# Kernel optimization log

Hardware: AMD Instinct MI355X
Metric: run time of the kernel (lower is better)

Reference implementation:

```python
import jax, jax.numpy as jnp
import numpy as np


def setup_inputs() -> dict:
    key = jax.random.key(0)
    k1, k2, k3, k4 = jax.random.split(key, 4)
    B, Nq, Nk, D = 8, 2048, 2048, 768
    return {
        "query": jax.random.normal(k1, (B, Nq, D), dtype=jnp.float32),
        "key": jax.random.normal(k2, (Nk, D), dtype=jnp.float32),
        "x": jax.random.normal(k3, (B, Nk, D), dtype=jnp.float32),
        "W": jax.random.normal(k4, (D, D), dtype=jnp.float32) * (1.0 / np.sqrt(D)),
        "b": jnp.zeros((D,), dtype=jnp.float32),
    }


def reference(query, key, x, W, b):
    # Linear projection: [B,Nq,dk] @ W^T + b -> [B,Nq,dq]
    query_proj = jnp.einsum("bqd,ed->bqe", query, W) + b
    # tensordot over dim_query: [B,Nq,dq] x [Nk,dq] -> [B,Nq,Nk]
    score = jnp.einsum("bqe,ke->bqk", query_proj, key)
    attn = jax.nn.softmax(score, axis=-1)
    # bmm: [B,Nq,Nk] @ [B,Nk,Dv] -> [B,Nq,Dv]
    out = jnp.einsum("bqk,bkd->bqd", attn, x)
    return (out, attn)
```

## Files before the change

### kernel.cpp

```cpp
#include <hip/hip_runtime.h>

typedef short s16x8 __attribute__((ext_vector_type(8)));
typedef _Float16 h16x8 __attribute__((ext_vector_type(8)));
typedef float f32x4 __attribute__((ext_vector_type(4)));

__device__ __forceinline__ unsigned short f2bf(float f) {
    unsigned int u = __builtin_bit_cast(unsigned int, f);
    u += 0x7FFFu + ((u >> 16) & 1u);
    return (unsigned short)(u >> 16);
}
__device__ __forceinline__ float bf2f(unsigned short h) {
    unsigned int u = ((unsigned int)h) << 16;
    return __builtin_bit_cast(float, u);
}
__device__ __forceinline__ unsigned short f2h(float f) {
    _Float16 h = (_Float16)f;
    return __builtin_bit_cast(unsigned short, h);
}
__device__ __forceinline__ float h2f(unsigned short u) {
    return (float)__builtin_bit_cast(_Float16, u);
}

__device__ __forceinline__ int swz(int row, int kbyte) {
    return (row * 64 + kbyte) ^ (((row >> 1) & 3) << 4);
}

__device__ __forceinline__ void gl16(const void* g, void* l) {
    __builtin_amdgcn_global_load_lds(
        (__attribute__((address_space(1))) void*)(g),
        (__attribute__((address_space(3))) void*)(l), 16, 0, 0);
}

#define STG(ptr, rowbase, tt, bufp, slot) do {                                      \
    gl16((ptr) + (long)((rowbase) + sl) * K + (tt) * 64 + koff,                     \
         &lds[bufp][slot][(unsigned)t * 8]);                                        \
    gl16((ptr) + (long)((rowbase) + 64 + sl) * K + (tt) * 64 + koff,                \
         &lds[bufp][slot][4096u + (unsigned)t * 8]);                                \
} while (0)

#define LDA(qi_) do {                                                               \
    const char* ba_ = (const char*)&lds[bp][qi_][0];                                \
    _Pragma("unroll")                                                               \
    for (int ks_ = 0; ks_ < 2; ++ks_)                                               \
        _Pragma("unroll")                                                           \
        for (int f_ = 0; f_ < 4; ++f_) {                                            \
            const int row_ = wm * 64 + f_ * 16 + lr;                                \
            af[ks_][f_] = *(const h16x8*)(ba_ + row_ * 128 +                        \
                            ((ks_ * 64 + kg16) ^ ((row_ & 7) << 4)));               \
        }                                                                           \
} while (0)

#define LDB(dst_, qj_) do {                                                         \
    const char* bb_ = (const char*)&lds[bp][2 + (qj_)][0];                          \
    _Pragma("unroll")                                                               \
    for (int ks_ = 0; ks_ < 2; ++ks_)                                               \
        _Pragma("unroll")                                                           \
        for (int g_ = 0; g_ < 2; ++g_) {                                            \
            const int row_ = wn * 32 + g_ * 16 + lr;                                \
            dst_[ks_][g_] = *(const h16x8*)(bb_ + row_ * 128 +                      \
                            ((ks_ * 64 + kg16) ^ ((row_ & 7) << 4)));               \
        }                                                                           \
} while (0)

#define SYNCV(VMSTR) do {                                                           \
    asm volatile("s_waitcnt vmcnt(" VMSTR ")" ::: "memory");                        \
    __builtin_amdgcn_s_barrier();                                                   \
    __builtin_amdgcn_sched_barrier(0);                                              \
} while (0)

#define MM(qi_, qj_, bfv_) do {                                                     \
    __builtin_amdgcn_s_setprio(1);                                                  \
    _Pragma("unroll")                                                               \
    for (int ks_ = 0; ks_ < 2; ++ks_)                                               \
        _Pragma("unroll")                                                           \
        for (int f_ = 0; f_ < 4; ++f_)                                              \
            _Pragma("unroll")                                                       \
            for (int g_ = 0; g_ < 2; ++g_)                                          \
                acc[qi_][qj_][f_][g_] = __builtin_amdgcn_mfma_f32_16x16x32_f16(     \
                    af[ks_][f_], bfv_[ks_][g_], acc[qi_][qj_][f_][g_], 0, 0, 0);    \
    __builtin_amdgcn_s_setprio(0);                                                  \
    __builtin_amdgcn_s_barrier();                                                   \
    __builtin_amdgcn_sched_barrier(0);                                              \
} while (0)

__global__ __launch_bounds__(512, 2) void score_8ph(
    const unsigned short* __restrict__ A, const unsigned short* __restrict__ Bm,
    const float* __restrict__ bias, float* __restrict__ C,
    int M, int N, int K, int nbx)
{
    __shared__ unsigned short lds[2][4][8192];

    const int bid = blockIdx.x;
    const int cpx = gridDim.x >> 3;
    const int sw  = (bid & 7) * cpx + (bid >> 3);
    const int m0 = (sw / nbx) * 256, n0 = (sw % nbx) * 256;

    const int t = threadIdx.x;
    const int l = t & 63, w = t >> 6;
    const int wm = w >> 2, wn = w & 3;
    const int lr = l & 15;
    const int kg16 = (l >> 4) * 16;

    const int sl   = w * 8 + (l >> 3);
    const int koff = ((l & 7) ^ (sl & 7)) * 8;

    h16x8 af[2][4], bf0[2][2], bf1[2][2];
    f32x4 acc[2][2][4][2];
    #pragma unroll
    for (int a = 0; a < 2; ++a)
        #pragma unroll
        for (int b = 0; b < 2; ++b)
            #pragma unroll
            for (int c = 0; c < 4; ++c)
                #pragma unroll
                for (int d = 0; d < 2; ++d)
                    acc[a][b][c][d] = (f32x4){0.f, 0.f, 0.f, 0.f};

    const int nt = K >> 6;

    STG(A,  m0,       0, 0, 0);
    STG(Bm, n0,       0, 0, 2);
    STG(Bm, n0 + 128, 0, 0, 3);
    STG(A,  m0 + 128, 0, 0, 1);
    STG(A,  m0,       1, 1, 0);
    STG(Bm, n0,       1, 1, 2);
    asm volatile("s_waitcnt vmcnt(8)" ::: "memory");
    __builtin_amdgcn_s_barrier();
    __builtin_amdgcn_sched_barrier(0);

    int tau = 0;
    for (; tau < nt - 2; ++tau) {
        const int bp = tau & 1;
        LDA(0); LDB(bf0, 0);
        STG(Bm, n0 + 128, tau + 1, bp ^ 1, 3);
        SYNCV("8");
        MM(0, 0, bf0);
        LDB(bf1, 1);
        STG(A, m0 + 128, tau + 1, bp ^ 1, 1);
        SYNCV("8");
        MM(0, 1, bf1);
        LDA(1);
        STG(A, m0, tau + 2, bp, 0);
        SYNCV("10");
        MM(1, 1, bf1);
        STG(Bm, n0, tau + 2, bp, 2);
        SYNCV("8");
        MM(1, 0, bf0);
    }
    {
        const int bp = tau & 1;
        LDA(0); LDB(bf0, 0);
        STG(Bm, n0 + 128, tau + 1, bp ^ 1, 3);
        SYNCV("8");
        MM(0, 0, bf0);
        LDB(bf1, 1);
        STG(A, m0 + 128, tau + 1, bp ^ 1, 1);
        SYNCV("8");
        MM(0, 1, bf1);
        LDA(1);
        SYNCV("8");
        MM(1, 1, bf1);
        SYNCV("4");
        MM(1, 0, bf0);
        ++tau;
    }
    {
        const int bp = tau & 1;
        LDA(0); LDB(bf0, 0);
        SYNCV("2");
        MM(0, 0, bf0);
        LDB(bf1, 1);
        SYNCV("0");
        MM(0, 1, bf1);
        LDA(1);
        SYNCV("0");
        MM(1, 1, bf1);
        SYNCV("0");
        MM(1, 0, bf0);
    }

    #pragma unroll
    for (int qi = 0; qi < 2; ++qi)
        #pragma unroll
        for (int qj = 0; qj < 2; ++qj)
            #pragma unroll
            for (int f = 0; f < 4; ++f)
                #pragma unroll
                for (int g = 0; g < 2; ++g) {
                    const int row = m0 + qi * 128 + wm * 64 + f * 16 + (l >> 4) * 4;
                    const int col = n0 + qj * 128 + wn * 32 + g * 16 + lr;
                    const float badd = bias[col];
                    #pragma unroll
                    for (int r = 0; r < 4; ++r)
                        C[(long)(row + r) * N + col] = acc[qi][qj][f][g][r] + badd;
                }
}

__global__ __launch_bounds__(256, 1) void pv_2ph(
    const unsigned short* __restrict__ A, const unsigned short* __restrict__ Bm,
    float* __restrict__ C, int M, int N, int K,
    long strideA, long strideB, long strideC)
{
    __shared__ unsigned short lds[2][2][128 * 64];

    const int bz = blockIdx.z;
    const unsigned short* Ab = A  + (long)bz * strideA;
    const unsigned short* Bb = Bm + (long)bz * strideB;
    float* Cb = C + (long)bz * strideC;
    const int m0 = blockIdx.x * 128, n0 = blockIdx.y * 128;

    const int t = threadIdx.x;
    const int l = t & 63, w = t >> 6;
    const int rm = (w >> 1) * 64, cn = (w & 1) * 64;
    const int lr = l & 15;
    const int kg16 = (l >> 4) * 16;

    const int jrow   = l >> 3;
    const int srcoff = ((l & 7) ^ jrow) << 3;

    const unsigned short* gA = Ab + (long)(m0 + jrow) * K + srcoff;
    const unsigned short* gB = Bb + (long)(n0 + jrow) * K + srcoff;

    f32x4 acc[4][4];
    #pragma unroll
    for (int i = 0; i < 4; ++i)
        #pragma unroll
        for (int j = 0; j < 4; ++j)
            acc[i][j] = (f32x4){0.f, 0.f, 0.f, 0.f};

    const int nt = K >> 6;
    #pragma unroll
    for (int i = 0; i < 4; ++i) {
        const int c = w * 4 + i;
        gl16(gA + (long)(8 * c) * K, &lds[0][0][c * 512]);
        gl16(gB + (long)(8 * c) * K, &lds[0][1][c * 512]);
    }
    __syncthreads();

    int p = 0;
    for (int it = 0; it < nt; ++it) {
        if (it + 1 < nt) {
            const unsigned short* nA = gA + (it + 1) * 64;
            const unsigned short* nB = gB + (it + 1) * 64;
            #pragma unroll
            for (int i = 0; i < 4; ++i) {
                const int c = w * 4 + i;
                gl16(nA + (long)(8 * c) * K, &lds[p ^ 1][0][c * 512]);
                gl16(nB + (long)(8 * c) * K, &lds[p ^ 1][1][c * 512]);
            }
        }
        const char* baseA = (const char*)&lds[p][0][0];
        const char* baseB = (const char*)&lds[p][1][0];
        h16x8 af[2][4], bf[2][4];
        #pragma unroll
        for (int ks = 0; ks < 2; ++ks)
            #pragma unroll
            for (int mi = 0; mi < 4; ++mi) {
                const int row = rm + mi * 16 + lr;
                af[ks][mi] = *(const h16x8*)(baseA + row * 128 +
                                ((ks * 64 + kg16) ^ ((row & 7) << 4)));
            }
        #pragma unroll
        for (int ks = 0; ks < 2; ++ks)
            #pragma unroll
            for (int nj = 0; nj < 4; ++nj) {
                const int row = cn + nj * 16 + lr;
                bf[ks][nj] = *(const h16x8*)(baseB + row * 128 +
                                ((ks * 64 + kg16) ^ ((row & 7) << 4)));
            }
        #pragma unroll
        for (int ks = 0; ks < 2; ++ks)
            #pragma unroll
            for (int mi = 0; mi < 4; ++mi)
                #pragma unroll
                for (int nj = 0; nj < 4; ++nj)
                    acc[mi][nj] = __builtin_amdgcn_mfma_f32_16x16x32_f16(
                        af[ks][mi], bf[ks][nj], acc[mi][nj], 0, 0, 0);
        __syncthreads();
        p ^= 1;
    }

    #pragma unroll
    for (int mi = 0; mi < 4; ++mi) {
        #pragma unroll
        for (int nj = 0; nj < 4; ++nj) {
            const int row = m0 + rm + mi * 16 + (l >> 4) * 4;
            const int col = n0 + cn + nj * 16 + lr;
            #pragma unroll
            for (int r = 0; r < 4; ++r)
                Cb[(long)(row + r) * N + col] = acc[mi][nj][r];
        }
    }
}

template<int SPLIT, bool TRANSB, bool BIAS>
__global__ __launch_bounds__(256, 1) void mfma_gemm(
    const float* __restrict__ A, const float* __restrict__ Bsrc,
    const float* __restrict__ bias, float* __restrict__ C,
    int M, int N, int K, long strideA, long strideB, long strideC)
{
    constexpr int NB = (SPLIT > 1) ? 2 : 1;
    __shared__ unsigned short sA[NB][128 * 32];
    __shared__ unsigned short sB[NB][128 * 32];

    const int t  = threadIdx.x;
    const int bz = blockIdx.z;
    const float* Ab = A    + (long)bz * strideA;
    const float* Bb = Bsrc + (long)bz * strideB;
    float*       Cb = C    + (long)bz * strideC;
    const int m0 = blockIdx.y * 128;
    const int n0 = blockIdx.x * 128;

    const int l  = t & 63, w = t >> 6;
    const int rm = (w >> 1) * 64;
    const int cn = (w & 1) * 64;
    const int lr = l & 15;
    const int kg = (l >> 4) * 16;

    const int srow = t >> 1;
    const int skh  = (t & 1) * 16;
    const int s_ = t & 15;
    const int kp = t >> 4;

    f32x4 acc[4][4];
    #pragma unroll
    for (int i = 0; i < 4; ++i)
        #pragma unroll
        for (int j = 0; j < 4; ++j)
            acc[i][j] = (f32x4){0.f, 0.f, 0.f, 0.f};

    for (int kt = 0; kt < K; kt += 32) {
        {
            const float* p = &Ab[(long)(m0 + srow) * K + kt + skh];
            float f[16];
            #pragma unroll
            for (int q = 0; q < 4; ++q) {
                const float4 v = *(const float4*)(p + 4 * q);
                f[4*q+0] = v.x; f[4*q+1] = v.y; f[4*q+2] = v.z; f[4*q+3] = v.w;
            }
            s16x8 h0, h1, l0, l1;
            #pragma unroll
            for (int q = 0; q < 8; ++q) {
                unsigned short h = f2bf(f[q]);      h0[q] = (short)h;
                if (SPLIT > 1) l0[q] = (short)f2bf(f[q] - bf2f(h));
                unsigned short g = f2bf(f[8 + q]);  h1[q] = (short)g;
                if (SPLIT > 1) l1[q] = (short)f2bf(f[8 + q] - bf2f(g));
            }
            *(s16x8*)((char*)sA[0] + swz(srow, skh * 2))      = h0;
            *(s16x8*)((char*)sA[0] + swz(srow, skh * 2 + 16)) = h1;
            if (SPLIT > 1) {
                *(s16x8*)((char*)sA[1] + swz(srow, skh * 2))      = l0;
                *(s16x8*)((char*)sA[1] + swz(srow, skh * 2 + 16)) = l1;
            }
        }
        if (!TRANSB) {
            const float* p = &Bb[(long)(n0 + srow) * K + kt + skh];
            float f[16];
            #pragma unroll
            for (int q = 0; q < 4; ++q) {
                const float4 v = *(const float4*)(p + 4 * q);
                f[4*q+0] = v.x; f[4*q+1] = v.y; f[4*q+2] = v.z; f[4*q+3] = v.w;
            }
            s16x8 h0, h1, l0, l1;
            #pragma unroll
            for (int q = 0; q < 8; ++q) {
                unsigned short h = f2bf(f[q]);      h0[q] = (short)h;
                if (SPLIT > 1) l0[q] = (short)f2bf(f[q] - bf2f(h));
                unsigned short g = f2bf(f[8 + q]);  h1[q] = (short)g;
                if (SPLIT > 1) l1[q] = (short)f2bf(f[8 + q] - bf2f(g));
            }
            *(s16x8*)((char*)sB[0] + swz(srow, skh * 2))      = h0;
            *(s16x8*)((char*)sB[0] + swz(srow, skh * 2 + 16)) = h1;
            if (SPLIT > 1) {
                *(s16x8*)((char*)sB[1] + swz(srow, skh * 2))      = l0;
                *(s16x8*)((char*)sB[1] + swz(srow, skh * 2 + 16)) = l1;
            }
        } else {
            const float* r0 = &Bb[(long)(kt + 2 * kp) * N + n0 + s_ * 8];
            const float* r1 = r0 + N;
            float a0[8], a1[8];
            {
                const float4 u0 = *(const float4*)(r0);
                const float4 u1 = *(const float4*)(r0 + 4);
                const float4 v0 = *(const float4*)(r1);
                const float4 v1 = *(const float4*)(r1 + 4);
                a0[0]=u0.x;a0[1]=u0.y;a0[2]=u0.z;a0[3]=u0.w;
                a0[4]=u1.x;a0[5]=u1.y;a0[6]=u1.z;a0[7]=u1.w;
                a1[0]=v0.x;a1[1]=v0.y;a1[2]=v0.z;a1[3]=v0.w;
                a1[4]=v1.x;a1[5]=v1.y;a1[6]=v1.z;a1[7]=v1.w;
            }
            #pragma unroll
            for (int j = 0; j < 8; ++j) {
                const int i  = (j + s_) & 7;
                const int nl = s_ * 8 + i;
                const unsigned int val =
                    (unsigned int)f2bf(a0[i]) | ((unsigned int)f2bf(a1[i]) << 16);
                *(unsigned int*)((char*)sB[0] + swz(nl, 4 * kp)) = val;
            }
        }
        __syncthreads();

        s16x8 ah[4], bh[4];
        #pragma unroll
        for (int mi = 0; mi < 4; ++mi)
            ah[mi] = *(const s16x8*)((const char*)sA[0] + swz(rm + mi * 16 + lr, kg));
        #pragma unroll
        for (int nj = 0; nj < 4; ++nj)
            bh[nj] = *(const s16x8*)((const char*)sB[0] + swz(cn + nj * 16 + lr, kg));
        #pragma unroll
        for (int mi = 0; mi < 4; ++mi)
            #pragma unroll
            for (int nj = 0; nj < 4; ++nj)
                acc[mi][nj] = __builtin_amdgcn_mfma_f32_16x16x32_bf16(
                    ah[mi], bh[nj], acc[mi][nj], 0, 0, 0);
        if (SPLIT > 1) {
            s16x8 al[4], bl[4];
            #pragma unroll
            for (int mi = 0; mi < 4; ++mi)
                al[mi] = *(const s16x8*)((const char*)sA[1] + swz(rm + mi * 16 + lr, kg));
            #pragma unroll
            for (int mi = 0; mi < 4; ++mi)
                #pragma unroll
                for (int nj = 0; nj < 4; ++nj)
                    acc[mi][nj] = __builtin_amdgcn_mfma_f32_16x16x32_bf16(
                        al[mi], bh[nj], acc[mi][nj], 0, 0, 0);
            #pragma unroll
            for (int nj = 0; nj < 4; ++nj)
                bl[nj] = *(const s16x8*)((const char*)sB[1] + swz(cn + nj * 16 + lr, kg));
            #pragma unroll
            for (int mi = 0; mi < 4; ++mi)
                #pragma unroll
                for (int nj = 0; nj < 4; ++nj)
                    acc[mi][nj] = __builtin_amdgcn_mfma_f32_16x16x32_bf16(
                        ah[mi], bl[nj], acc[mi][nj], 0, 0, 0);
        }
        __syncthreads();
    }

    #pragma unroll
    for (int mi = 0; mi < 4; ++mi) {
        #pragma unroll
        for (int nj = 0; nj < 4; ++nj) {
            const int row = m0 + rm + mi * 16 + (l >> 4) * 4;
            const int col = n0 + cn + nj * 16 + lr;
            const float badd = BIAS ? bias[col] : 0.f;
            #pragma unroll
            for (int r = 0; r < 4; ++r)
                Cb[(long)(row + r) * N + col] = acc[mi][nj][r] + badd;
        }
    }
}

__global__ __launch_bounds__(256, 1) void score_gemm(
    const unsigned short* __restrict__ Ah, const unsigned short* __restrict__ Al,
    const unsigned short* __restrict__ Bh, const unsigned short* __restrict__ Bl,
    const float* __restrict__ bias, float* __restrict__ C,
    int M, int N, int K, int nbx)
{
    __shared__ unsigned short sAh[128 * 32];
    __shared__ unsigned short sBh[128 * 32];
    __shared__ unsigned short sAl[128 * 32];
    __shared__ unsigned short sBl[128 * 32];

    const int bid = blockIdx.x;
    const int cpx = gridDim.x >> 3;
    const int sw  = (bid & 7) * cpx + (bid >> 3);
    const int mb  = sw / nbx, nb = sw % nbx;
    const int m0 = mb * 128, n0 = nb * 128;

    const int t = threadIdx.x;
    const int l = t & 63, w = t >> 6;
    const int rm = (w >> 1) * 64;
    const int cn = (w & 1) * 64;
    const int lr = l & 15;
    const int kg = (l >> 4) * 16;

    const int r0 = 2 * w, r1 = 2 * w + 1;
    const int rowS0 = 16 * r0 + (l >> 2);
    const int rowS1 = 16 * r1 + (l >> 2);
    const int h0 = (l & 3) ^ ((rowS0 >> 1) & 3);
    const int h1 = (l & 3) ^ ((rowS1 >> 1) & 3);

    const unsigned short* gAh0 = Ah + (long)(m0 + rowS0) * K + 8 * h0;
    const unsigned short* gAh1 = Ah + (long)(m0 + rowS1) * K + 8 * h1;
    const unsigned short* gAl0 = Al + (long)(m0 + rowS0) * K + 8 * h0;
    const unsigned short* gAl1 = Al + (long)(m0 + rowS1) * K + 8 * h1;
    const unsigned short* gBh0 = Bh + (long)(n0 + rowS0) * K + 8 * h0;
    const unsigned short* gBh1 = Bh + (long)(n0 + rowS1) * K + 8 * h1;
    const unsigned short* gBl0 = Bl + (long)(n0 + rowS0) * K + 8 * h0;
    const unsigned short* gBl1 = Bl + (long)(n0 + rowS1) * K + 8 * h1;

    unsigned short* dA0 = &sAh[r0 * 512];
    unsigned short* dA1 = &sAh[r1 * 512];
    unsigned short* dAl0 = &sAl[r0 * 512];
    unsigned short* dAl1 = &sAl[r1 * 512];
    unsigned short* dB0 = &sBh[r0 * 512];
    unsigned short* dB1 = &sBh[r1 * 512];
    unsigned short* dBl0 = &sBl[r0 * 512];
    unsigned short* dBl1 = &sBl[r1 * 512];

    f32x4 acc[4][4];
    #pragma unroll
    for (int i = 0; i < 4; ++i)
        #pragma unroll
        for (int j = 0; j < 4; ++j)
            acc[i][j] = (f32x4){0.f, 0.f, 0.f, 0.f};

    const int nk = K >> 5;
    for (int it = 0; it < nk; ++it) {
        gl16(gAh0, dA0);  gl16(gAh1, dA1);
        gl16(gBh0, dB0);  gl16(gBh1, dB1);
        gl16(gAl0, dAl0); gl16(gAl1, dAl1);
        gl16(gBl0, dBl0); gl16(gBl1, dBl1);
        gAh0 += 32; gAh1 += 32; gAl0 += 32; gAl1 += 32;
        gBh0 += 32; gBh1 += 32; gBl0 += 32; gBl1 += 32;
        __syncthreads();

        s16x8 ah[4], bh[4];
        #pragma unroll
        for (int mi = 0; mi < 4; ++mi)
            ah[mi] = *(const s16x8*)((const char*)sAh + swz(rm + mi * 16 + lr, kg));
        #pragma unroll
        for (int nj = 0; nj < 4; ++nj)
            bh[nj] = *(const s16x8*)((const char*)sBh + swz(cn + nj * 16 + lr, kg));
        #pragma unroll
        for (int mi = 0; mi < 4; ++mi)
            #pragma unroll
            for (int nj = 0; nj < 4; ++nj)
                acc[mi][nj] = __builtin_amdgcn_mfma_f32_16x16x32_bf16(
                    ah[mi], bh[nj], acc[mi][nj], 0, 0, 0);
        s16x8 al[4], bl[4];
        #pragma unroll
        for (int mi = 0; mi < 4; ++mi)
            al[mi] = *(const s16x8*)((const char*)sAl + swz(rm + mi * 16 + lr, kg));
        #pragma unroll
        for (int mi = 0; mi < 4; ++mi)
            #pragma unroll
            for (int nj = 0; nj < 4; ++nj)
                acc[mi][nj] = __builtin_amdgcn_mfma_f32_16x16x32_bf16(
                    al[mi], bh[nj], acc[mi][nj], 0, 0, 0);
        #pragma unroll
        for (int nj = 0; nj < 4; ++nj)
            bl[nj] = *(const s16x8*)((const char*)sBl + swz(cn + nj * 16 + lr, kg));
        #pragma unroll
        for (int mi = 0; mi < 4; ++mi)
            #pragma unroll
            for (int nj = 0; nj < 4; ++nj)
                acc[mi][nj] = __builtin_amdgcn_mfma_f32_16x16x32_bf16(
                    ah[mi], bl[nj], acc[mi][nj], 0, 0, 0);
        __syncthreads();
    }

    #pragma unroll
    for (int mi = 0; mi < 4; ++mi) {
        #pragma unroll
        for (int nj = 0; nj < 4; ++nj) {
            const int row = m0 + rm + mi * 16 + (l >> 4) * 4;
            const int col = n0 + cn + nj * 16 + lr;
            const float badd = bias[col];
            #pragma unroll
            for (int r = 0; r < 4; ++r)
                C[(long)(row + r) * N + col] = acc[mi][nj][r] + badd;
        }
    }
}

__global__ __launch_bounds__(256, 1) void out_gemm(
    const float* __restrict__ A32, const unsigned short* __restrict__ B16,
    float* __restrict__ C, int M, int N, int K,
    long strideA, long strideB, long strideC)
{
    __shared__ unsigned short sA[128 * 32];
    __shared__ unsigned short sB[128 * 32];

    const int bz = blockIdx.z;
    const float* Ab = A32 + (long)bz * strideA;
    const unsigned short* Bb = B16 + (long)bz * strideB;
    float* Cb = C + (long)bz * strideC;
    const int m0 = blockIdx.x * 128;
    const int n0 = blockIdx.y * 128;

    const int t = threadIdx.x;
    const int l = t & 63, w = t >> 6;
    const int rm = (w >> 1) * 64;
    const int cn = (w & 1) * 64;
    const int lr = l & 15;
    const int kg = (l >> 4) * 16;

    const int r0 = 2 * w, r1 = 2 * w + 1;
    const int rowS0 = 16 * r0 + (l >> 2);
    const int rowS1 = 16 * r1 + (l >> 2);
    const int h0 = (l & 3) ^ ((rowS0 >> 1) & 3);
    const int h1 = (l & 3) ^ ((rowS1 >> 1) & 3);
    const unsigned short* gB0 = Bb + (long)(n0 + rowS0) * K + 8 * h0;
    const unsigned short* gB1 = Bb + (long)(n0 + rowS1) * K + 8 * h1;
    unsigned short* dB0 = &sB[r0 * 512];
    unsigned short* dB1 = &sB[r1 * 512];

    const int srow = t >> 1;
    const int skh  = (t & 1) * 16;
    const float* gA = &Ab[(long)(m0 + srow) * K + skh];

    f32x4 acc[4][4];
    #pragma unroll
    for (int i = 0; i < 4; ++i)
        #pragma unroll
        for (int j = 0; j < 4; ++j)
            acc[i][j] = (f32x4){0.f, 0.f, 0.f, 0.f};

    const int nk = K >> 5;
    for (int it = 0; it < nk; ++it) {
        gl16(gB0, dB0); gl16(gB1, dB1);
        gB0 += 32; gB1 += 32;
        {
            float f[16];
            #pragma unroll
            for (int q = 0; q < 4; ++q) {
                const float4 v = *(const float4*)(gA + 4 * q);
                f[4*q+0] = v.x; f[4*q+1] = v.y; f[4*q+2] = v.z; f[4*q+3] = v.w;
            }
            gA += 32;
            s16x8 v0, v1;
            #pragma unroll
            for (int q = 0; q < 8; ++q) {
                v0[q] = (short)f2bf(f[q]);
                v1[q] = (short)f2bf(f[8 + q]);
            }
            *(s16x8*)((char*)sA + swz(srow, skh * 2))      = v0;
            *(s16x8*)((char*)sA + swz(srow, skh * 2 + 16)) = v1;
        }
        __syncthreads();

        s16x8 ah[4], bh[4];
        #pragma unroll
        for (int mi = 0; mi < 4; ++mi)
            ah[mi] = *(const s16x8*)((const char*)sA + swz(rm + mi * 16 + lr, kg));
        #pragma unroll
        for (int nj = 0; nj < 4; ++nj)
            bh[nj] = *(const s16x8*)((const char*)sB + swz(cn + nj * 16 + lr, kg));
        #pragma unroll
        for (int mi = 0; mi < 4; ++mi)
            #pragma unroll
            for (int nj = 0; nj < 4; ++nj)
                acc[mi][nj] = __builtin_amdgcn_mfma_f32_16x16x32_bf16(
                    ah[mi], bh[nj], acc[mi][nj], 0, 0, 0);
        __syncthreads();
    }

    #pragma unroll
    for (int mi = 0; mi < 4; ++mi) {
        #pragma unroll
        for (int nj = 0; nj < 4; ++nj) {
            const int row = m0 + rm + mi * 16 + (l >> 4) * 4;
            const int col = n0 + cn + nj * 16 + lr;
            #pragma unroll
            for (int r = 0; r < 4; ++r)
                Cb[(long)(row + r) * N + col] = acc[mi][nj][r];
        }
    }
}

template<int MODE>
__global__ __launch_bounds__(256) void transpose64(
    const float* __restrict__ in, void* __restrict__ outv,
    int R, int Cc, long sIn, long sOut)
{
    __shared__ float tl[64][65];
    const int z = blockIdx.z;
    const float* ib = in + (long)z * sIn;
    const int r0 = blockIdx.x * 64, c0 = blockIdx.y * 64;
    const int t = threadIdx.x;
    const int lrr = t >> 4, lc = (t & 15) * 4;
    #pragma unroll
    for (int p = 0; p < 4; ++p) {
        const float4 v = *(const float4*)&ib[(long)(r0 + lrr + 16 * p) * Cc + c0 + lc];
        tl[lrr + 16 * p][lc + 0] = v.x; tl[lrr + 16 * p][lc + 1] = v.y;
        tl[lrr + 16 * p][lc + 2] = v.z; tl[lrr + 16 * p][lc + 3] = v.w;
    }
    __syncthreads();
    #pragma unroll
    for (int p = 0; p < 4; ++p) {
        const int orow = c0 + lrr + 16 * p;
        const int ocol = r0 + lc;
        const float a = tl[lc + 0][lrr + 16 * p];
        const float b = tl[lc + 1][lrr + 16 * p];
        const float c = tl[lc + 2][lrr + 16 * p];
        const float d = tl[lc + 3][lrr + 16 * p];
        if (MODE == 1) {
            ushort4 u = { f2bf(a), f2bf(b), f2bf(c), f2bf(d) };
            *(ushort4*)((unsigned short*)outv + (long)z * sOut + (long)orow * R + ocol) = u;
        } else if (MODE == 2) {
            ushort4 u = { f2h(a), f2h(b), f2h(c), f2h(d) };
            *(ushort4*)((unsigned short*)outv + (long)z * sOut + (long)orow * R + ocol) = u;
        } else {
            float4 u = { a, b, c, d };
            *(float4*)((float*)outv + (long)z * sOut + (long)orow * R + ocol) = u;
        }
    }
}

__global__ __launch_bounds__(256) void convert_hilo(
    const float* __restrict__ src, unsigned short* __restrict__ hi,
    unsigned short* __restrict__ lo, long n8)
{
    for (long i = (long)blockIdx.x * blockDim.x + threadIdx.x; i < n8;
         i += (long)gridDim.x * blockDim.x) {
        const float4 a = *(const float4*)&src[i * 8];
        const float4 b = *(const float4*)&src[i * 8 + 4];
        const float f[8] = { a.x, a.y, a.z, a.w, b.x, b.y, b.z, b.w };
        s16x8 h, lv;
        #pragma unroll
        for (int q = 0; q < 8; ++q) {
            const unsigned short hh = f2bf(f[q]);
            h[q]  = (short)hh;
            lv[q] = (short)f2bf(f[q] - bf2f(hh));
        }
        *(s16x8*)&hi[i * 8] = h;
        *(s16x8*)&lo[i * 8] = lv;
    }
}

__global__ __launch_bounds__(256) void convert_q_ilv(
    const float* __restrict__ src, unsigned short* __restrict__ dst,
    int kd8, long n8)
{
    const int Kd = kd8 * 8;
    for (long i = (long)blockIdx.x * blockDim.x + threadIdx.x; i < n8;
         i += (long)gridDim.x * blockDim.x) {
        const long row = i / kd8;
        const int  col = (int)(i - row * kd8) * 8;
        const float4 a = *(const float4*)&src[i * 8];
        const float4 b = *(const float4*)&src[i * 8 + 4];
        const float f[8] = { a.x, a.y, a.z, a.w, b.x, b.y, b.z, b.w };
        s16x8 h, lv;
        #pragma unroll
        for (int q = 0; q < 8; ++q) {
            const unsigned short hh = f2h(f[q]);
            h[q]  = (short)hh;
            lv[q] = (short)f2h(f[q] - h2f(hh));
        }
        unsigned short* dr = dst + row * (long)(2 * Kd);
        *(s16x8*)&dr[col]      = h;
        *(s16x8*)&dr[Kd + col] = lv;
    }
}

__global__ __launch_bounds__(256) void convert_kw_dup(
    const float* __restrict__ src, unsigned short* __restrict__ dst,
    int kd8, long n8)
{
    const int Kd = kd8 * 8;
    for (long i = (long)blockIdx.x * blockDim.x + threadIdx.x; i < n8;
         i += (long)gridDim.x * blockDim.x) {
        const long row = i / kd8;
        const int  col = (int)(i - row * kd8) * 8;
        const float4 a = *(const float4*)&src[i * 8];
        const float4 b = *(const float4*)&src[i * 8 + 4];
        const float f[8] = { a.x, a.y, a.z, a.w, b.x, b.y, b.z, b.w };
        s16x8 h;
        #pragma unroll
        for (int q = 0; q < 8; ++q) h[q] = (short)f2h(f[q]);
        unsigned short* dr = dst + row * (long)(2 * Kd);
        *(s16x8*)&dr[col]      = h;
        *(s16x8*)&dr[Kd + col] = h;
    }
}

__global__ __launch_bounds__(256) void bk_dot(
    const float* __restrict__ key, const float* __restrict__ b,
    float* __restrict__ bk, int D)
{
    const int row = blockIdx.x * 4 + (threadIdx.x >> 6);
    const int l = threadIdx.x & 63;
    const float* kr = key + (long)row * D;
    float s = 0.f;
    for (int e = l; e < D; e += 64) s += kr[e] * b[e];
    #pragma unroll
    for (int off = 32; off > 0; off >>= 1) s += __shfl_xor(s, off);
    if (l == 0) bk[row] = s;
}

__global__ __launch_bounds__(256) void softmax_f16(
    float* __restrict__ S, unsigned short* __restrict__ S16, int cols)
{
    const long row = blockIdx.x;
    float* p = S + row * (long)cols;
    unsigned short* p16 = S16 + row * (long)cols;
    const int t = threadIdx.x;
    const int wid = t >> 6;
    const int base = t * 8;

    const float4 a = *(const float4*)&p[base];
    const float4 b = *(const float4*)&p[base + 4];
    float vals[8] = { a.x, a.y, a.z, a.w, b.x, b.y, b.z, b.w };
    float m = -INFINITY;
    #pragma unroll
    for (int i = 0; i < 8; ++i) m = fmaxf(m, vals[i]);
    #pragma unroll
    for (int off = 32; off > 0; off >>= 1)
        m = fmaxf(m, __shfl_xor(m, off));
    __shared__ float smax[4], ssum[4];
    if ((t & 63) == 0) smax[wid] = m;
    __syncthreads();
    m = fmaxf(fmaxf(smax[0], smax[1]), fmaxf(smax[2], smax[3]));

    float s = 0.f;
    #pragma unroll
    for (int i = 0; i < 8; ++i) {
        vals[i] = __expf(vals[i] - m);
        s += vals[i];
    }
    #pragma unroll
    for (int off = 32; off > 0; off >>= 1)
        s += __shfl_xor(s, off);
    if ((t & 63) == 0) ssum[wid] = s;
    __syncthreads();
    s = (ssum[0] + ssum[1]) + (ssum[2] + ssum[3]);
    const float inv = 1.0f / s;

    float4 o0, o1;
    o0.x = vals[0]*inv; o0.y = vals[1]*inv; o0.z = vals[2]*inv; o0.w = vals[3]*inv;
    o1.x = vals[4]*inv; o1.y = vals[5]*inv; o1.z = vals[6]*inv; o1.w = vals[7]*inv;
    *(float4*)&p[base]     = o0;
    *(float4*)&p[base + 4] = o1;
    s16x8 h;
    h[0]=(short)f2h(o0.x); h[1]=(short)f2h(o0.y); h[2]=(short)f2h(o0.z); h[3]=(short)f2h(o0.w);
    h[4]=(short)f2h(o1.x); h[5]=(short)f2h(o1.y); h[6]=(short)f2h(o1.z); h[7]=(short)f2h(o1.w);
    *(s16x8*)&p16[base] = h;
}

__global__ __launch_bounds__(256) void softmax_rows(float* __restrict__ S, int cols)
{
    const long row = blockIdx.x;
    float* p = S + row * (long)cols;
    const int t = threadIdx.x;
    const int wid = t >> 6;

    float vals[8];
    float m = -INFINITY;
    #pragma unroll
    for (int i = 0; i < 8; ++i) {
        vals[i] = p[t + i * 256];
        m = fmaxf(m, vals[i]);
    }
    #pragma unroll
    for (int off = 32; off > 0; off >>= 1)
        m = fmaxf(m, __shfl_xor(m, off));
    __shared__ float smax[4], ssum[4];
    if ((t & 63) == 0) smax[wid] = m;
    __syncthreads();
    m = fmaxf(fmaxf(smax[0], smax[1]), fmaxf(smax[2], smax[3]));

    float s = 0.f;
    #pragma unroll
    for (int i = 0; i < 8; ++i) {
        vals[i] = __expf(vals[i] - m);
        s += vals[i];
    }
    #pragma unroll
    for (int off = 32; off > 0; off >>= 1)
        s += __shfl_xor(s, off);
    if ((t & 63) == 0) ssum[wid] = s;
    __syncthreads();
    s = (ssum[0] + ssum[1]) + (ssum[2] + ssum[3]);
    const float inv = 1.0f / s;
    #pragma unroll
    for (int i = 0; i < 8; ++i)
        p[t + i * 256] = vals[i] * inv;
}

extern "C" void kernel_launch(void* const* d_in, const int* in_sizes, int n_in,
                              void* d_out, int out_size, void* d_ws, size_t ws_size,
                              hipStream_t stream)
{
    const float* query = (const float*)d_in[0];
    const float* key   = (const float*)d_in[1];
    const float* x     = (const float*)d_in[2];
    const float* W     = (const float*)d_in[3];
    const float* bias  = (const float*)d_in[4];

    const int D  = in_sizes[4];
    const int Nk = in_sizes[1] / D;
    const int B  = in_sizes[2] / (Nk * D);
    const int Nq = in_sizes[0] / (B * D);

    float* out  = (float*)d_out;
    float* attn = out + (long)B * Nq * D;

    const long nQ  = (long)B * Nq * D;
    const long nKW = (long)Nk * D;
    const long nX  = (long)B * Nk * D;
    const int  M   = B * Nq;
    const int  K2  = 2 * D;

    const size_t xTb    = (size_t)nX * 2;
    const size_t kwDupB = (size_t)Nk * K2 * 2;
    const size_t bkB    = (size_t)Nk * 4;
    const size_t atb1   = (size_t)Nq * Nk * 2;
    const size_t fixedB = xTb + kwDupB + bkB;
    const size_t qLob   = (size_t)nQ * 2;
    const size_t wsMid  = xTb + qLob;

    int g = 0;
    if (ws_size >= fixedB + 2 * atb1) {
        g = (int)((ws_size - fixedB) / atb1);
        if (g > B) g = B;
    }

    if (g >= 2) {
        unsigned short* qIlv  = (unsigned short*)out;
        unsigned short* xT     = (unsigned short*)d_ws;
        unsigned short* kwDup  = (unsigned short*)((char*)d_ws + xTb);
        float*          bk     = (float*)((char*)d_ws + xTb + kwDupB);
        unsigned short* attn16 = (unsigned short*)((char*)d_ws + fixedB);
        float* Wt  = attn;
        float* KWf = attn + 1048576;

        dim3 gtw(D / 64, D / 64, 1);
        transpose64<0><<<gtw, 256, 0, stream>>>(W, Wt, D, D, 0L, 0L);
        dim3 gkw(D / 128, Nk / 128, 1);
        mfma_gemm<3, false, false><<<gkw, 256, 0, stream>>>(
            key, Wt, nullptr, KWf, Nk, D, D, 0L, 0L, 0L);
        convert_kw_dup<<<768, 256, 0, stream>>>(KWf, kwDup, D / 8, nKW / 8);
        bk_dot<<<Nk / 4, 256, 0, stream>>>(key, bias, bk, D);
        convert_q_ilv<<<2048, 256, 0, stream>>>(query, qIlv, D / 8, nQ / 8);
        dim3 gtx(Nk / 64, D / 64, B);
        transpose64<2><<<gtx, 256, 0, stream>>>(
            x, xT, Nk, D, (long)Nk * D, (long)D * Nk);

        const int nbx = Nk / 256;
        const int nwg = (M / 256) * nbx;
        score_8ph<<<nwg, 512, 0, stream>>>(
            qIlv, kwDup, bk, attn, M, Nk, K2, nbx);

        for (int b0 = 0; b0 < B; b0 += g) {
            const int gb = (b0 + g <= B) ? g : (B - b0);
            softmax_f16<<<gb * Nq, 256, 0, stream>>>(
                attn + (long)b0 * Nq * Nk, attn16, Nk);
            dim3 go(Nq / 128, D / 128, gb);
            pv_2ph<<<go, 256, 0, stream>>>(
                attn16, xT + (long)b0 * D * Nk, out + (long)b0 * Nq * D,
                Nq, D, Nk, (long)Nq * Nk, (long)D * Nk, (long)Nq * D);
        }
    } else if (ws_size >= wsMid) {
        unsigned short* q_hi  = (unsigned short*)out;
        unsigned short* KW_hi = q_hi + nQ;
        unsigned short* KW_lo = KW_hi + nKW;
        float*          bk    = (float*)(KW_lo + nKW);
        unsigned short* q_lo  = (unsigned short*)d_ws;
        unsigned short* xT    = q_lo + nQ;
        float* Wt  = attn;
        float* KWf = attn + 1048576;

        dim3 gtw(D / 64, D / 64, 1);
        transpose64<0><<<gtw, 256, 0, stream>>>(W, Wt, D, D, 0L, 0L);
        dim3 gkw(D / 128, Nk / 128, 1);
        mfma_gemm<3, false, false><<<gkw, 256, 0, stream>>>(
            key, Wt, nullptr, KWf, Nk, D, D, 0L, 0L, 0L);
        convert_hilo<<<768, 256, 0, stream>>>(KWf, KW_hi, KW_lo, nKW / 8);
        bk_dot<<<Nk / 4, 256, 0, stream>>>(key, bias, bk, D);
        convert_hilo<<<2048, 256, 0, stream>>>(query, q_hi, q_lo, nQ / 8);
        dim3 gtx(Nk / 64, D / 64, B);
        transpose64<1><<<gtx, 256, 0, stream>>>(
            x, xT, Nk, D, (long)Nk * D, (long)D * Nk);
        const int nbx = Nk / 128;
        const int nwg = (B * Nq / 128) * nbx;
        score_gemm<<<nwg, 256, 0, stream>>>(
            q_hi, q_lo, KW_hi, KW_lo, bk, attn, B * Nq, Nk, D, nbx);
        softmax_rows<<<B * Nq, 256, 0, stream>>>(attn, Nk);
        dim3 go(Nq / 128, D / 128, B);
        out_gemm<<<go, 256, 0, stream>>>(
            attn, xT, out, Nq, D, Nk, (long)Nq * Nk, (long)D * Nk, (long)Nq * D);
    } else {
        float* qp = out;
        dim3 g1(D / 128, (B * Nq) / 128, 1);
        mfma_gemm<3, false, true><<<g1, 256, 0, stream>>>(
            query, W, bias, qp, B * Nq, D, D, 0L, 0L, 0L);
        dim3 g2(Nk / 128, Nq / 128, B);
        mfma_gemm<3, false, false><<<g2, 256, 0, stream>>>(
            qp, key, nullptr, attn, Nq, Nk, D, (long)Nq * D, 0L, (long)Nq * Nk);
        softmax_rows<<<B * Nq, 256, 0, stream>>>(attn, Nk);
        dim3 g4(D / 128, Nq / 128, B);
        mfma_gemm<1, true, false><<<g4, 256, 0, stream>>>(
            attn, x, nullptr, out, Nq, D, Nk, (long)Nq * Nk, (long)Nk * D, (long)Nq * D);
    }
}
```

Before: 336.8 us.

## Emit fp16 scores, fuse softmax in place, and process batches in two groups

Adds a new path, used when the workspace is large enough and B==8. It runs the score GEMM in two 4-batch groups and writes the scores as fp16 into a workspace slot instead of fp32 into attn. A new softmax kernel reads the fp16 slot, writes fp32 attn, and overwrites the slot with fp16 probabilities for the PV GEMM. This replaces the fp32 score write plus fp32 read in softmax with smaller fp16 traffic. The score kernel's global-load pipeline is also re-timed: next-stage loads are issued earlier and there is one vmcnt wait per iteration instead of a wait at each phase. The risk is reduced precision from rounding scores to fp16 before the softmax, and possible load/LDS-buffer hazards under the new prefetch ordering.

Measured after the change: 311.4 us. 1.08x faster.

```diff
diff --git a/kernel.cpp b/kernel.cpp
--- a/kernel.cpp
+++ b/kernel.cpp
@@ -62,8 +62,7 @@
         }                                                                           \
 } while (0)
 
-#define SYNCV(VMSTR) do {                                                           \
-    asm volatile("s_waitcnt vmcnt(" VMSTR ")" ::: "memory");                        \
+#define BARR() do {                                                                 \
     __builtin_amdgcn_s_barrier();                                                   \
     __builtin_amdgcn_sched_barrier(0);                                              \
 } while (0)
@@ -83,9 +82,10 @@
     __builtin_amdgcn_sched_barrier(0);                                              \
 } while (0)
 
+template<int F16OUT>
 __global__ __launch_bounds__(512, 2) void score_8ph(
     const unsigned short* __restrict__ A, const unsigned short* __restrict__ Bm,
-    const float* __restrict__ bias, float* __restrict__ C,
+    const float* __restrict__ bias, void* __restrict__ Cv,
     int M, int N, int K, int nbx)
 {
     __shared__ unsigned short lds[2][4][8192];
@@ -124,58 +124,59 @@
     STG(A,  m0 + 128, 0, 0, 1);
     STG(A,  m0,       1, 1, 0);
     STG(Bm, n0,       1, 1, 2);
+    STG(Bm, n0 + 128, 1, 1, 3);
+    STG(A,  m0 + 128, 1, 1, 1);
     asm volatile("s_waitcnt vmcnt(8)" ::: "memory");
-    __builtin_amdgcn_s_barrier();
-    __builtin_amdgcn_sched_barrier(0);
+    BARR();
 
     int tau = 0;
     for (; tau < nt - 2; ++tau) {
         const int bp = tau & 1;
         LDA(0); LDB(bf0, 0);
-        STG(Bm, n0 + 128, tau + 1, bp ^ 1, 3);
-        SYNCV("8");
+        BARR();
         MM(0, 0, bf0);
         LDB(bf1, 1);
-        STG(A, m0 + 128, tau + 1, bp ^ 1, 1);
-        SYNCV("8");
+        STG(A, m0, tau + 2, bp, 0);
+        BARR();
         MM(0, 1, bf1);
         LDA(1);
-        STG(A, m0, tau + 2, bp, 0);
-        SYNCV("10");
+        STG(Bm, n0, tau + 2, bp, 2);
+        BARR();
         MM(1, 1, bf1);
-        STG(Bm, n0, tau + 2, bp, 2);
-        SYNCV("8");
+        STG(Bm, n0 + 128, tau + 2, bp, 3);
+        STG(A,  m0 + 128, tau + 2, bp, 1);
+        asm volatile("s_waitcnt vmcnt(8)" ::: "memory");
+        BARR();
         MM(1, 0, bf0);
     }
     {
         const int bp = tau & 1;
         LDA(0); LDB(bf0, 0);
-        STG(Bm, n0 + 128, tau + 1, bp ^ 1, 3);
-        SYNCV("8");
+        BARR();
         MM(0, 0, bf0);
         LDB(bf1, 1);
-        STG(A, m0 + 128, tau + 1, bp ^ 1, 1);
-        SYNCV("8");
+        BARR();
         MM(0, 1, bf1);
         LDA(1);
-        SYNCV("8");
+        BARR();
         MM(1, 1, bf1);
-        SYNCV("4");
+        asm volatile("s_waitcnt vmcnt(0)" ::: "memory");
+        BARR();
         MM(1, 0, bf0);
         ++tau;
     }
     {
         const int bp = tau & 1;
         LDA(0); LDB(bf0, 0);
-        SYNCV("2");
+        BARR();
         MM(0, 0, bf0);
         LDB(bf1, 1);
-        SYNCV("0");
+        BARR();
         MM(0, 1, bf1);
         LDA(1);
-        SYNCV("0");
+        BARR();
         MM(1, 1, bf1);
-        SYNCV("0");
+        BARR();
         MM(1, 0, bf0);
     }
 
@@ -190,9 +191,18 @@
                     const int row = m0 + qi * 128 + wm * 64 + f * 16 + (l >> 4) * 4;
                     const int col = n0 + qj * 128 + wn * 32 + g * 16 + lr;
                     const float badd = bias[col];
-                    #pragma unroll
-                    for (int r = 0; r < 4; ++r)
-                        C[(long)(row + r) * N + col] = acc[qi][qj][f][g][r] + badd;
+                    if (F16OUT) {
+                        unsigned short* C = (unsigned short*)Cv;
+                        #pragma unroll
+                        for (int r = 0; r < 4; ++r)
+                            C[(long)(row + r) * N + col] =
+                                f2h(acc[qi][qj][f][g][r] + badd);
+                    } else {
+                        float* C = (float*)Cv;
+                        #pragma unroll
+                        for (int r = 0; r < 4; ++r)
+                            C[(long)(row + r) * N + col] = acc[qi][qj][f][g][r] + badd;
+                    }
                 }
 }
 
@@ -780,6 +790,56 @@
     if (l == 0) bk[row] = s;
 }
 
+__global__ __launch_bounds__(256) void softmax_h16(
+    unsigned short* __restrict__ L16, float* __restrict__ Afp, int cols)
+{
+    const long row = blockIdx.x;
+    unsigned short* pl = L16 + row * (long)cols;
+    float* pf = Afp + row * (long)cols;
+    const int t = threadIdx.x;
+    const int wid = t >> 6;
+    const int base = t * 8;
+
+    const s16x8 hv = *(const s16x8*)&pl[base];
+    float vals[8];
+    #pragma unroll
+    for (int i = 0; i < 8; ++i) vals[i] = h2f((unsigned short)hv[i]);
+    float m = -INFINITY;
+    #pragma unroll
+    for (int i = 0; i < 8; ++i) m = fmaxf(m, vals[i]);
+    #pragma unroll
+    for (int off = 32; off > 0; off >>= 1)
+        m = fmaxf(m, __shfl_xor(m, off));
+    __shared__ float smax[4], ssum[4];
+    if ((t & 63) == 0) smax[wid] = m;
+    __syncthreads();
+    m = fmaxf(fmaxf(smax[0], smax[1]), fmaxf(smax[2], smax[3]));
+
+    float s = 0.f;
+    #pragma unroll
+    for (int i = 0; i < 8; ++i) {
+        vals[i] = __expf(vals[i] - m);
+        s += vals[i];
+    }
+    #pragma unroll
+    for (int off = 32; off > 0; off >>= 1)
+        s += __shfl_xor(s, off);
+    if ((t & 63) == 0) ssum[wid] = s;
+    __syncthreads();
+    s = (ssum[0] + ssum[1]) + (ssum[2] + ssum[3]);
+    const float inv = 1.0f / s;
+
+    float4 o0, o1;
+    o0.x = vals[0]*inv; o0.y = vals[1]*inv; o0.z = vals[2]*inv; o0.w = vals[3]*inv;
+    o1.x = vals[4]*inv; o1.y = vals[5]*inv; o1.z = vals[6]*inv; o1.w = vals[7]*inv;
+    *(float4*)&pf[base]     = o0;
+    *(float4*)&pf[base + 4] = o1;
+    s16x8 h;
+    h[0]=(short)f2h(o0.x); h[1]=(short)f2h(o0.y); h[2]=(short)f2h(o0.z); h[3]=(short)f2h(o0.w);
+    h[4]=(short)f2h(o1.x); h[5]=(short)f2h(o1.y); h[6]=(short)f2h(o1.z); h[7]=(short)f2h(o1.w);
+    *(s16x8*)&pl[base] = h;
+}
+
 __global__ __launch_bounds__(256) void softmax_f16(
     float* __restrict__ S, unsigned short* __restrict__ S16, int cols)
 {
@@ -900,6 +960,7 @@
     const size_t fixedB = xTb + kwDupB + bkB;
     const size_t qLob   = (size_t)nQ * 2;
     const size_t wsMid  = xTb + qLob;
+    const size_t wsF16  = fixedB + 4 * atb1;
 
     int g = 0;
     if (ws_size >= fixedB + 2 * atb1) {
@@ -907,12 +968,12 @@
         if (g > B) g = B;
     }
 
-    if (g >= 2) {
+    if (ws_size >= wsF16 && B == 8) {
         unsigned short* qIlv  = (unsigned short*)out;
-        unsigned short* xT     = (unsigned short*)d_ws;
-        unsigned short* kwDup  = (unsigned short*)((char*)d_ws + xTb);
-        float*          bk     = (float*)((char*)d_ws + xTb + kwDupB);
-        unsigned short* attn16 = (unsigned short*)((char*)d_ws + fixedB);
+        unsigned short* xT    = (unsigned short*)d_ws;
+        unsigned short* kwDup = (unsigned short*)((char*)d_ws + xTb);
+        float*          bk    = (float*)((char*)d_ws + xTb + kwDupB);
+        unsigned short* slot  = (unsigned short*)((char*)d_ws + fixedB);
         float* Wt  = attn;
         float* KWf = attn + 1048576;
 
@@ -929,8 +990,42 @@
             x, xT, Nk, D, (long)Nk * D, (long)D * Nk);
 
         const int nbx = Nk / 256;
+        for (int grp = 0; grp < 2; ++grp) {
+            const int b0 = grp * 4;
+            const int nwg = (4 * Nq / 256) * nbx;
+            score_8ph<1><<<nwg, 512, 0, stream>>>(
+                qIlv + (long)b0 * Nq * K2, kwDup, bk, slot, 4 * Nq, Nk, K2, nbx);
+            softmax_h16<<<4 * Nq, 256, 0, stream>>>(
+                slot, attn + (long)b0 * Nq * Nk, Nk);
+            dim3 go(Nq / 128, D / 128, 4);
+            pv_2ph<<<go, 256, 0, stream>>>(
+                slot, xT + (long)b0 * D * Nk, out + (long)b0 * Nq * D,
+                Nq, D, Nk, (long)Nq * Nk, (long)D * Nk, (long)Nq * D);
+        }
+    } else if (g >= 2) {
+        unsigned short* qIlv  = (unsigned short*)out;
+        unsigned short* xT     = (unsigned short*)d_ws;
+        unsigned short* kwDup  = (unsigned short*)((char*)d_ws + xTb);
+        float*          bk     = (float*)((char*)d_ws + xTb + kwDupB);
+        unsigned short* attn16 = (unsigned short*)((char*)d_ws + fixedB);
+        float* Wt  = attn;
+        float* KWf = attn + 1048576;
+
+        dim3 gtw(D / 64, D / 64, 1);
+        transpose64<0><<<gtw, 256, 0, stream>>>(W, Wt, D, D, 0L, 0L);
+        dim3 gkw(D / 128, Nk / 128, 1);
+        mfma_gemm<3, false, false><<<gkw, 256, 0, stream>>>(
+            key, Wt, nullptr, KWf, Nk, D, D, 0L, 0L, 0L);
+        convert_kw_dup<<<768, 256, 0, stream>>>(KWf, kwDup, D / 8, nKW / 8);
+        bk_dot<<<Nk / 4, 256, 0, stream>>>(key, bias, bk, D);
+        convert_q_ilv<<<2048, 256, 0, stream>>>(query, qIlv, D / 8, nQ / 8);
+        dim3 gtx(Nk / 64, D / 64, B);
+        transpose64<2><<<gtx, 256, 0, stream>>>(
+            x, xT, Nk, D, (long)Nk * D, (long)D * Nk);
+
+        const int nbx = Nk / 256;
         const int nwg = (M / 256) * nbx;
-        score_8ph<<<nwg, 512, 0, stream>>>(
+        score_8ph<0><<<nwg, 512, 0, stream>>>(
             qIlv, kwDup, bk, attn, M, Nk, K2, nbx);
 
         for (int b0 = 0; b0 < B; b0 += g) {
@@ -957,7 +1052,7 @@
         dim3 gkw(D / 128, Nk / 128, 1);
         mfma_gemm<3, false, false><<<gkw, 256, 0, stream>>>(
             key, Wt, nullptr, KWf, Nk, D, D, 0L, 0L, 0L);
-        convert_hilo<<<768, 256, 0, stream>>>(KWf, KW_hi, KW_lo, nKW / 8);
+        convert_hilo<<<768, 256, 0, stream>>>(KWf, (unsigned short*)KW_hi, KW_lo, nKW / 8);
         bk_dot<<<Nk / 4, 256, 0, stream>>>(key, bias, bk, D);
         convert_hilo<<<2048, 256, 0, stream>>>(query, q_hi, q_lo, nQ / 8);
         dim3 gtx(Nk / 64, D / 64, B);
```
